# Performance work log

Measured on AMD Instinct MI355X. Metric: run time of the kernel, lower is better.

The kernel has to match this reference:

```python
import jax, jax.numpy as jnp
import numpy as np

N_NODES = 50000
N_USERS = 10000
N_STATE = 1024
N_T1 = 2048
N_T2 = 2048
N_EDGES = 4096


def setup_inputs() -> dict:
    key = jax.random.key(0)
    ks = jax.random.split(key, 10)
    d = N_STATE
    s_u = jax.random.normal(ks[0], (N_USERS, d), jnp.float32)
    x = jax.random.normal(ks[1], (N_NODES, d), jnp.float32)
    # Deterministic graph on which the original torch code is well-defined:
    # POI node 0 has one outgoing edge (edge 0) to tail node 1.
    # Tail node 1 receives edges from heads [0, 2, 3, ..., N_EDGES] in edge order,
    # so list-order in the torch loop aligns with edge-index order.
    heads = np.concatenate([[0], np.arange(2, N_EDGES + 1)]).astype(np.int64)
    tails = np.ones(N_EDGES, dtype=np.int64)
    edge_index = jnp.asarray(np.stack([heads, tails]))
    edge_attr = jax.random.normal(ks[2], (N_EDGES, d), jnp.float32)
    T = jax.random.normal(ks[3], (N_T1, N_T2), jnp.float32)
    u = lambda k, s: jax.random.uniform(k, s, jnp.float32, -1.0, 1.0)
    W_u = u(ks[4], (d, 1))
    W_p = u(ks[5], (d, 1))
    W_T_1 = u(ks[6], (d, N_T1))
    W_T_2 = u(ks[7], (N_T2, 1))
    b_T = u(ks[8], (d, 1))
    W_p_ = u(ks[9], (1, d))
    return dict(s_u=s_u, x=x, edge_attr=edge_attr, T=T, W_u=W_u, W_p=W_p,
                W_T_1=W_T_1, W_T_2=W_T_2, b_T=b_T, W_p_=W_p_,
                edge_index=edge_index, user_index=7, POI_index=0)


def reference(s_u, x, edge_attr, T, W_u, W_p, W_T_1, W_T_2, b_T, W_p_,
              edge_index, user_index, POI_index):
    N, d = x.shape
    heads, tails = edge_index[0], edge_index[1]
    # temporal context vector: sigmoid(W_T_1 @ T @ W_T_2 + b_T), shape (d,)
    t_vec = jax.nn.sigmoid(W_T_1 @ T @ W_T_2 + b_T)[:, 0]
    cur_user = s_u[user_index]   # (d,)
    cur_POI = x[POI_index]       # (d,)
    # user update: u' = sigmoid(u + W_u * (h_P . T'))
    s_u = s_u.at[user_index].set(
        jax.nn.sigmoid(cur_user + W_u[:, 0] * jnp.dot(cur_POI, t_vec)))
    # visited POI update: h' = sigmoid(h + W_p * (u . T'))
    new_POI = jax.nn.sigmoid(cur_POI + W_p[:, 0] * jnp.dot(cur_user, t_vec))
    x = x.at[POI_index].set(new_POI)
    # tail entities of the visited POI: x[tail] = new_POI + edge_attr[e]
    rel_mask = heads == POI_index
    dummy = jnp.zeros((1, d), x.dtype)
    tgt = jnp.where(rel_mask, tails, N)  # route masked-out edges to dummy row
    x = jnp.concatenate([x, dummy], 0).at[tgt].set(new_POI[None, :] + edge_attr)[:N]
    # neighboring POIs: edges whose tail is in the tail set; replicate the original
    # neigh_rel[POI_index] = False / neigh_index.remove(POI_index) pair, which by
    # construction both drop the edge at position POI_index.
    is_tail = jnp.zeros((N + 1,), bool).at[tgt].set(True)[:N]
    neigh_mask = is_tail[tails].at[POI_index].set(False)  # (E,)
    h_emb = x[heads]                        # (E, d), tail-updated embeddings
    scal = (h_emb - edge_attr) @ W_p_[0]    # (E,)  W_p_ . (x[head] - r)
    vals = jax.nn.sigmoid(h_emb + scal[:, None])
    tgt2 = jnp.where(neigh_mask, heads, N)
    x = jnp.concatenate([x, dummy], 0).at[tgt2].set(vals)[:N]
    return (s_u, x)
```

## Files before the change

### kernel.cpp

```cpp
#include <hip/hip_runtime.h>
#include <math.h>
#include <limits.h>

#define D 1024

__device__ __forceinline__ float sigmoidf_(float v) {
    return 1.0f / (1.0f + expf(-v));
}

__device__ __forceinline__ float block_reduce_sum256(float v) {
    #pragma unroll
    for (int off = 32; off; off >>= 1) v += __shfl_down(v, off, 64);
    __shared__ float sm[4];
    int lane = threadIdx.x & 63, w = threadIdx.x >> 6;
    if (lane == 0) sm[w] = v;
    __syncthreads();
    float s = sm[0] + sm[1] + sm[2] + sm[3];
    __syncthreads();
    return s;
}

__device__ __forceinline__ float block_reduce_sum1024(float v) {
    #pragma unroll
    for (int off = 32; off; off >>= 1) v += __shfl_down(v, off, 64);
    __shared__ float sm[16];
    int lane = threadIdx.x & 63, w = threadIdx.x >> 6;
    if (lane == 0) sm[w] = v;
    __syncthreads();
    float s = 0.f;
    #pragma unroll
    for (int i = 0; i < 16; i++) s += sm[i];
    __syncthreads();
    return s;
}

__global__ void k_matvec_T(const float* __restrict__ T,
                           const float* __restrict__ w,
                           float* __restrict__ tmp) {
    int row = blockIdx.x;
    const float4* Tr = (const float4*)(T + (size_t)row * 2048);
    const float4* wv = (const float4*)w;
    float acc = 0.f;
    for (int i = threadIdx.x; i < 512; i += 256) {
        float4 a = Tr[i], b = wv[i];
        acc += a.x * b.x + a.y * b.y + a.z * b.z + a.w * b.w;
    }
    float s = block_reduce_sum256(acc);
    if (threadIdx.x == 0) tmp[row] = s;
}

__global__ void k_tvec(const float* __restrict__ W_T_1,
                       const float* __restrict__ tmp,
                       const float* __restrict__ b_T,
                       float* __restrict__ t_vec) {
    int row = blockIdx.x;
    const float4* Wr = (const float4*)(W_T_1 + (size_t)row * 2048);
    const float4* tv = (const float4*)tmp;
    float acc = 0.f;
    for (int i = threadIdx.x; i < 512; i += 256) {
        float4 a = Wr[i], b = tv[i];
        acc += a.x * b.x + a.y * b.y + a.z * b.z + a.w * b.w;
    }
    float s = block_reduce_sum256(acc);
    if (threadIdx.x == 0) t_vec[row] = sigmoidf_(s + b_T[row]);
}

__global__ void k_setup(const int* __restrict__ edge_index,
                        const float* __restrict__ x,
                        const float* __restrict__ s_u,
                        const float* __restrict__ t_vec,
                        const float* __restrict__ W_u,
                        const float* __restrict__ W_p,
                        const int* __restrict__ user_ptr,
                        const int* __restrict__ POI_ptr,
                        int* __restrict__ tail_edge,
                        int* __restrict__ neigh_edge,
                        float* __restrict__ new_user,
                        float* __restrict__ new_POI, int E) {
    const int tid = threadIdx.x;
    const int POI = POI_ptr[0], user = user_ptr[0];

    for (int e = tid; e < E; e += 1024) {
        int h = edge_index[e], t = edge_index[E + e];
        tail_edge[h] = -1;  tail_edge[t] = -1;
        neigh_edge[h] = -1; neigh_edge[t] = -1;
    }
    if (tid == 0) { tail_edge[POI] = -1; neigh_edge[POI] = -1; }
    __syncthreads();

    for (int e = tid; e < E; e += 1024)
        if (edge_index[e] == POI) atomicMax(&tail_edge[edge_index[E + e]], e);
    __syncthreads();

    for (int e = tid; e < E; e += 1024) {
        if (e == POI) continue;
        int t = edge_index[E + e];
        int te = atomicMax(&tail_edge[t], INT_MIN);
        if (te >= 0) atomicMax(&neigh_edge[edge_index[e]], e);
    }
    __syncthreads();

    float xv = x[(size_t)POI * D + tid];
    float uv = s_u[(size_t)user * D + tid];
    float tv = t_vec[tid];
    float dotP = block_reduce_sum1024(xv * tv);
    float dotU = block_reduce_sum1024(uv * tv);
    new_user[tid] = sigmoidf_(uv + W_u[tid] * dotP);
    new_POI[tid]  = sigmoidf_(xv + W_p[tid] * dotU);
}

__global__ void k_copy_all(const float4* __restrict__ su,
                           const float4* __restrict__ xx,
                           float4* __restrict__ out,
                           int n4_su, int n4_total) {
    int i = blockIdx.x * blockDim.x + threadIdx.x;
    int stride = gridDim.x * blockDim.x;
    for (; i < n4_total; i += stride)
        out[i] = (i < n4_su) ? su[i] : xx[i - n4_su];
}

__global__ void k_fixup(const int* __restrict__ edge_index,
                        const float* __restrict__ edge_attr,
                        const float* __restrict__ x,
                        const float* __restrict__ Wp_row,
                        const float* __restrict__ new_user,
                        const float* __restrict__ new_POI,
                        const int* __restrict__ tail_edge,
                        const int* __restrict__ neigh_edge,
                        const int* __restrict__ user_ptr,
                        const int* __restrict__ POI_ptr,
                        float* __restrict__ out_su,
                        float* __restrict__ out_x, int E) {
    const int e = blockIdx.x;
    const int tid = threadIdx.x;
    const int POI = POI_ptr[0];
    const float4* np_ = (const float4*)new_POI;

    if (e == E) {
        int user = user_ptr[0];
        ((float4*)(out_su + (size_t)user * D))[tid] =
            ((const float4*)new_user)[tid];
        if (tail_edge[POI] < 0 && neigh_edge[POI] < 0)
            ((float4*)(out_x + (size_t)POI * D))[tid] = np_[tid];
        return;
    }

    const int h = edge_index[e], t = edge_index[E + e];

    if (h == POI && tail_edge[t] == e && neigh_edge[t] < 0) {
        const float4* ea = (const float4*)(edge_attr + (size_t)e * D);
        float4 a = np_[tid], b = ea[tid];
        ((float4*)(out_x + (size_t)t * D))[tid] =
            make_float4(a.x + b.x, a.y + b.y, a.z + b.z, a.w + b.w);
    }

    if (e != POI && tail_edge[t] >= 0 && neigh_edge[h] == e) {
        float4 hv;
        int be = tail_edge[h];
        if (be >= 0) {
            const float4* eb = (const float4*)(edge_attr + (size_t)be * D);
            float4 a = np_[tid], b = eb[tid];
            hv = make_float4(a.x + b.x, a.y + b.y, a.z + b.z, a.w + b.w);
        } else if (h == POI) {
            hv = np_[tid];
        } else {
            hv = ((const float4*)(x + (size_t)h * D))[tid];
        }
        const float4* ea = (const float4*)(edge_attr + (size_t)e * D);
        float4 ev = ea[tid];
        float4 w = ((const float4*)Wp_row)[tid];
        float acc = (hv.x - ev.x) * w.x + (hv.y - ev.y) * w.y +
                    (hv.z - ev.z) * w.z + (hv.w - ev.w) * w.w;
        float scal = block_reduce_sum256(acc);
        float4 o;
        o.x = sigmoidf_(hv.x + scal);
        o.y = sigmoidf_(hv.y + scal);
        o.z = sigmoidf_(hv.z + scal);
        o.w = sigmoidf_(hv.w + scal);
        ((float4*)(out_x + (size_t)h * D))[tid] = o;
    }
}

extern "C" void kernel_launch(void* const* d_in, const int* in_sizes, int n_in,
                              void* d_out, int out_size, void* d_ws, size_t ws_size,
                              hipStream_t stream) {
    const float* s_u       = (const float*)d_in[0];
    const float* x         = (const float*)d_in[1];
    const float* edge_attr = (const float*)d_in[2];
    const float* T         = (const float*)d_in[3];
    const float* W_u       = (const float*)d_in[4];
    const float* W_p       = (const float*)d_in[5];
    const float* W_T_1     = (const float*)d_in[6];
    const float* W_T_2     = (const float*)d_in[7];
    const float* b_T       = (const float*)d_in[8];
    const float* W_p_      = (const float*)d_in[9];
    const int*   edge_index = (const int*)d_in[10];
    const int*   user_ptr   = (const int*)d_in[11];
    const int*   POI_ptr    = (const int*)d_in[12];

    const int E       = in_sizes[10] / 2;
    const int N_users = in_sizes[0] / D;
    const int N       = in_sizes[1] / D;

    float* out_su = (float*)d_out;
    float* out_x  = out_su + (size_t)N_users * D;

    float* ws_f      = (float*)d_ws;
    float* tmp       = ws_f;
    float* t_vec     = ws_f + 2048;
    float* new_user  = ws_f + 3072;
    float* new_POI   = ws_f + 4096;
    int*   tail_edge = (int*)(ws_f + 5120);
    int*   neigh_edge = tail_edge + N;

    k_matvec_T<<<2048, 256, 0, stream>>>(T, W_T_2, tmp);
    k_tvec<<<1024, 256, 0, stream>>>(W_T_1, tmp, b_T, t_vec);
    k_setup<<<1, 1024, 0, stream>>>(edge_index, x, s_u, t_vec, W_u, W_p,
                                    user_ptr, POI_ptr, tail_edge, neigh_edge,
                                    new_user, new_POI, E);

    const int n4_su = (int)((size_t)N_users * D / 4);
    const int n4_total = n4_su + (int)((size_t)N * D / 4);
    k_copy_all<<<4096, 256, 0, stream>>>((const float4*)s_u, (const float4*)x,
                                         (float4*)d_out, n4_su, n4_total);

    k_fixup<<<E + 1, 256, 0, stream>>>(edge_index, edge_attr, x, W_p_,
                                       new_user, new_POI, tail_edge, neigh_edge,
                                       user_ptr, POI_ptr, out_su, out_x, E);
}
```

Before: 125.5 us.

## Fuse copy and fixup into a per-row mega kernel, overlap graph setup with matvec

Replaces the separate full-array copy kernel and per-edge fixup kernel with one kernel that handles each output row: it either streams the row with nontemporal loads and stores or computes the updated user, POI, tail or neighbour value in place. This avoids writing special rows twice and removes a launch. The graph-index construction moves into an extra block of the first matvec kernel, and the tail/neighbour tables are initialised with a memset. The POI and user dot products are folded into the t_vec kernel as partial products that each updating block reduces itself. The costs are a per-block branch over 60k rows, redundant recomputation of new_POI in every special row, and a full 2N-int memset.

```diff
diff --git a/kernel.cpp b/kernel.cpp
--- a/kernel.cpp
+++ b/kernel.cpp
@@ -3,6 +3,8 @@
 #include <limits.h>
 
 #define D 1024
+
+typedef float f32x4 __attribute__((ext_vector_type(4)));
 
 __device__ __forceinline__ float sigmoidf_(float v) {
     return 1.0f / (1.0f + expf(-v));
@@ -20,165 +22,153 @@
     return s;
 }
 
-__device__ __forceinline__ float block_reduce_sum1024(float v) {
-    #pragma unroll
-    for (int off = 32; off; off >>= 1) v += __shfl_down(v, off, 64);
-    __shared__ float sm[16];
-    int lane = threadIdx.x & 63, w = threadIdx.x >> 6;
-    if (lane == 0) sm[w] = v;
+__global__ void k_pre(const float* __restrict__ T,
+                      const float* __restrict__ w,
+                      float* __restrict__ tmp,
+                      const int* __restrict__ edge_index,
+                      const int* __restrict__ POI_ptr,
+                      int* __restrict__ tail_edge,
+                      int* __restrict__ neigh_edge,
+                      int n_rows, int E, int t4 ) {
+    const int b = blockIdx.x;
+    const int tid = threadIdx.x;
+    if (b < n_rows) {
+        const float4* Tr = (const float4*)(T + (size_t)b * (size_t)(t4 * 4));
+        const float4* wv = (const float4*)w;
+        float acc = 0.f;
+        for (int i = tid; i < t4; i += 256) {
+            float4 a = Tr[i], c = wv[i];
+            acc += a.x * c.x + a.y * c.y + a.z * c.z + a.w * c.w;
+        }
+        float s = block_reduce_sum256(acc);
+        if (tid == 0) tmp[b] = s;
+        return;
+    }
+    const int POI = POI_ptr[0];
+    for (int e = tid; e < E; e += 256)
+        if (edge_index[e] == POI) atomicMax(&tail_edge[edge_index[E + e]], e);
     __syncthreads();
-    float s = 0.f;
-    #pragma unroll
-    for (int i = 0; i < 16; i++) s += sm[i];
-    __syncthreads();
-    return s;
-}
-
-__global__ void k_matvec_T(const float* __restrict__ T,
-                           const float* __restrict__ w,
-                           float* __restrict__ tmp) {
-    int row = blockIdx.x;
-    const float4* Tr = (const float4*)(T + (size_t)row * 2048);
-    const float4* wv = (const float4*)w;
-    float acc = 0.f;
-    for (int i = threadIdx.x; i < 512; i += 256) {
-        float4 a = Tr[i], b = wv[i];
-        acc += a.x * b.x + a.y * b.y + a.z * b.z + a.w * b.w;
-    }
-    float s = block_reduce_sum256(acc);
-    if (threadIdx.x == 0) tmp[row] = s;
-}
-
-__global__ void k_tvec(const float* __restrict__ W_T_1,
-                       const float* __restrict__ tmp,
-                       const float* __restrict__ b_T,
-                       float* __restrict__ t_vec) {
-    int row = blockIdx.x;
-    const float4* Wr = (const float4*)(W_T_1 + (size_t)row * 2048);
+    for (int e = tid; e < E; e += 256) {
+        if (e == POI) continue;
+        int te = atomicMax(&tail_edge[edge_index[E + e]], INT_MIN);
+        if (te >= 0) atomicMax(&neigh_edge[edge_index[e]], e);
+    }
+}
+
+__global__ void k_tvec2(const float* __restrict__ W_T_1,
+                        const float* __restrict__ tmp,
+                        const float* __restrict__ b_T,
+                        const float* __restrict__ x,
+                        const float* __restrict__ s_u,
+                        const int* __restrict__ user_ptr,
+                        const int* __restrict__ POI_ptr,
+                        float* __restrict__ pu_P,
+                        float* __restrict__ pu_U,
+                        int k4 ) {
+    const int row = blockIdx.x;
+    const float4* Wr = (const float4*)(W_T_1 + (size_t)row * (size_t)(k4 * 4));
     const float4* tv = (const float4*)tmp;
     float acc = 0.f;
-    for (int i = threadIdx.x; i < 512; i += 256) {
-        float4 a = Wr[i], b = tv[i];
-        acc += a.x * b.x + a.y * b.y + a.z * b.z + a.w * b.w;
+    for (int i = threadIdx.x; i < k4; i += 256) {
+        float4 a = Wr[i], c = tv[i];
+        acc += a.x * c.x + a.y * c.y + a.z * c.z + a.w * c.w;
     }
     float s = block_reduce_sum256(acc);
-    if (threadIdx.x == 0) t_vec[row] = sigmoidf_(s + b_T[row]);
-}
-
-__global__ void k_setup(const int* __restrict__ edge_index,
-                        const float* __restrict__ x,
-                        const float* __restrict__ s_u,
-                        const float* __restrict__ t_vec,
-                        const float* __restrict__ W_u,
-                        const float* __restrict__ W_p,
-                        const int* __restrict__ user_ptr,
-                        const int* __restrict__ POI_ptr,
-                        int* __restrict__ tail_edge,
-                        int* __restrict__ neigh_edge,
-                        float* __restrict__ new_user,
-                        float* __restrict__ new_POI, int E) {
+    if (threadIdx.x == 0) {
+        float t = sigmoidf_(s + b_T[row]);
+        pu_P[row] = x[(size_t)POI_ptr[0] * D + row] * t;
+        pu_U[row] = s_u[(size_t)user_ptr[0] * D + row] * t;
+    }
+}
+
+__global__ void k_mega(const float* __restrict__ s_u,
+                       const float* __restrict__ x,
+                       const float* __restrict__ edge_attr,
+                       const float* __restrict__ W_u,
+                       const float* __restrict__ W_p,
+                       const float* __restrict__ Wp_row,
+                       const int* __restrict__ user_ptr,
+                       const int* __restrict__ POI_ptr,
+                       const int* __restrict__ tail_edge,
+                       const int* __restrict__ neigh_edge,
+                       const float* __restrict__ pu_P,
+                       const float* __restrict__ pu_U,
+                       float* __restrict__ out,
+                       int N_users, int E) {
+    const int r = blockIdx.x;
     const int tid = threadIdx.x;
-    const int POI = POI_ptr[0], user = user_ptr[0];
-
-    for (int e = tid; e < E; e += 1024) {
-        int h = edge_index[e], t = edge_index[E + e];
-        tail_edge[h] = -1;  tail_edge[t] = -1;
-        neigh_edge[h] = -1; neigh_edge[t] = -1;
-    }
-    if (tid == 0) { tail_edge[POI] = -1; neigh_edge[POI] = -1; }
-    __syncthreads();
-
-    for (int e = tid; e < E; e += 1024)
-        if (edge_index[e] == POI) atomicMax(&tail_edge[edge_index[E + e]], e);
-    __syncthreads();
-
-    for (int e = tid; e < E; e += 1024) {
-        if (e == POI) continue;
-        int t = edge_index[E + e];
-        int te = atomicMax(&tail_edge[t], INT_MIN);
-        if (te >= 0) atomicMax(&neigh_edge[edge_index[e]], e);
-    }
-    __syncthreads();
-
-    float xv = x[(size_t)POI * D + tid];
-    float uv = s_u[(size_t)user * D + tid];
-    float tv = t_vec[tid];
-    float dotP = block_reduce_sum1024(xv * tv);
-    float dotU = block_reduce_sum1024(uv * tv);
-    new_user[tid] = sigmoidf_(uv + W_u[tid] * dotP);
-    new_POI[tid]  = sigmoidf_(xv + W_p[tid] * dotU);
-}
-
-__global__ void k_copy_all(const float4* __restrict__ su,
-                           const float4* __restrict__ xx,
-                           float4* __restrict__ out,
-                           int n4_su, int n4_total) {
-    int i = blockIdx.x * blockDim.x + threadIdx.x;
-    int stride = gridDim.x * blockDim.x;
-    for (; i < n4_total; i += stride)
-        out[i] = (i < n4_su) ? su[i] : xx[i - n4_su];
-}
-
-__global__ void k_fixup(const int* __restrict__ edge_index,
-                        const float* __restrict__ edge_attr,
-                        const float* __restrict__ x,
-                        const float* __restrict__ Wp_row,
-                        const float* __restrict__ new_user,
-                        const float* __restrict__ new_POI,
-                        const int* __restrict__ tail_edge,
-                        const int* __restrict__ neigh_edge,
-                        const int* __restrict__ user_ptr,
-                        const int* __restrict__ POI_ptr,
-                        float* __restrict__ out_su,
-                        float* __restrict__ out_x, int E) {
-    const int e = blockIdx.x;
-    const int tid = threadIdx.x;
+
+    if (r < N_users) {
+        if (r == user_ptr[0]) {
+            float4 pp = ((const float4*)pu_P)[tid];
+            float dotP = block_reduce_sum256(pp.x + pp.y + pp.z + pp.w);
+            float4 uv = ((const float4*)(s_u + (size_t)r * D))[tid];
+            float4 wu = ((const float4*)W_u)[tid];
+            float4 o;
+            o.x = sigmoidf_(uv.x + wu.x * dotP);
+            o.y = sigmoidf_(uv.y + wu.y * dotP);
+            o.z = sigmoidf_(uv.z + wu.z * dotP);
+            o.w = sigmoidf_(uv.w + wu.w * dotP);
+            ((float4*)(out + (size_t)r * D))[tid] = o;
+        } else {
+            const f32x4* src = (const f32x4*)(s_u + (size_t)r * D);
+            f32x4* dst = (f32x4*)(out + (size_t)r * D);
+            f32x4 v = __builtin_nontemporal_load(&src[tid]);
+            __builtin_nontemporal_store(v, &dst[tid]);
+        }
+        return;
+    }
+
+    const int j = r - N_users;
+    const int ne = neigh_edge[j];
+    const int te = tail_edge[j];
     const int POI = POI_ptr[0];
-    const float4* np_ = (const float4*)new_POI;
-
-    if (e == E) {
-        int user = user_ptr[0];
-        ((float4*)(out_su + (size_t)user * D))[tid] =
-            ((const float4*)new_user)[tid];
-        if (tail_edge[POI] < 0 && neigh_edge[POI] < 0)
-            ((float4*)(out_x + (size_t)POI * D))[tid] = np_[tid];
-        return;
-    }
-
-    const int h = edge_index[e], t = edge_index[E + e];
-
-    if (h == POI && tail_edge[t] == e && neigh_edge[t] < 0) {
-        const float4* ea = (const float4*)(edge_attr + (size_t)e * D);
-        float4 a = np_[tid], b = ea[tid];
-        ((float4*)(out_x + (size_t)t * D))[tid] =
-            make_float4(a.x + b.x, a.y + b.y, a.z + b.z, a.w + b.w);
-    }
-
-    if (e != POI && tail_edge[t] >= 0 && neigh_edge[h] == e) {
-        float4 hv;
-        int be = tail_edge[h];
-        if (be >= 0) {
-            const float4* eb = (const float4*)(edge_attr + (size_t)be * D);
-            float4 a = np_[tid], b = eb[tid];
-            hv = make_float4(a.x + b.x, a.y + b.y, a.z + b.z, a.w + b.w);
-        } else if (h == POI) {
-            hv = np_[tid];
-        } else {
-            hv = ((const float4*)(x + (size_t)h * D))[tid];
-        }
-        const float4* ea = (const float4*)(edge_attr + (size_t)e * D);
-        float4 ev = ea[tid];
-        float4 w = ((const float4*)Wp_row)[tid];
-        float acc = (hv.x - ev.x) * w.x + (hv.y - ev.y) * w.y +
-                    (hv.z - ev.z) * w.z + (hv.w - ev.w) * w.w;
-        float scal = block_reduce_sum256(acc);
-        float4 o;
-        o.x = sigmoidf_(hv.x + scal);
-        o.y = sigmoidf_(hv.y + scal);
-        o.z = sigmoidf_(hv.z + scal);
-        o.w = sigmoidf_(hv.w + scal);
-        ((float4*)(out_x + (size_t)h * D))[tid] = o;
-    }
+
+    if (ne < 0 && te < 0 && j != POI) {
+        const f32x4* src = (const f32x4*)(x + (size_t)j * D);
+        f32x4* dst = (f32x4*)(out + (size_t)r * D);
+        f32x4 v = __builtin_nontemporal_load(&src[tid]);
+        __builtin_nontemporal_store(v, &dst[tid]);
+        return;
+    }
+
+    float4 uu = ((const float4*)pu_U)[tid];
+    float dotU = block_reduce_sum256(uu.x + uu.y + uu.z + uu.w);
+    float4 xp = ((const float4*)(x + (size_t)POI * D))[tid];
+    float4 wp = ((const float4*)W_p)[tid];
+    float4 np;
+    np.x = sigmoidf_(xp.x + wp.x * dotU);
+    np.y = sigmoidf_(xp.y + wp.y * dotU);
+    np.z = sigmoidf_(xp.z + wp.z * dotU);
+    np.w = sigmoidf_(xp.w + wp.w * dotU);
+
+    float4 hv;
+    if (te >= 0) {
+        float4 b = ((const float4*)(edge_attr + (size_t)te * D))[tid];
+        hv = make_float4(np.x + b.x, np.y + b.y, np.z + b.z, np.w + b.w);
+    } else if (j == POI) {
+        hv = np;
+    } else {
+        hv = ((const float4*)(x + (size_t)j * D))[tid];
+    }
+
+    float4* dst = (float4*)(out + (size_t)r * D);
+    if (ne < 0) {
+        dst[tid] = hv;
+        return;
+    }
+
+    float4 ev = ((const float4*)(edge_attr + (size_t)ne * D))[tid];
+    float4 w = ((const float4*)Wp_row)[tid];
+    float acc = (hv.x - ev.x) * w.x + (hv.y - ev.y) * w.y +
+                (hv.z - ev.z) * w.z + (hv.w - ev.w) * w.w;
+    float scal = block_reduce_sum256(acc);
+    float4 o;
+    o.x = sigmoidf_(hv.x + scal);
+    o.y = sigmoidf_(hv.y + scal);
+    o.z = sigmoidf_(hv.z + scal);
+    o.w = sigmoidf_(hv.w + scal);
+    dst[tid] = o;
 }
 
 extern "C" void kernel_launch(void* const* d_in, const int* in_sizes, int n_in,
@@ -201,30 +191,24 @@
     const int E       = in_sizes[10] / 2;
     const int N_users = in_sizes[0] / D;
     const int N       = in_sizes[1] / D;
-
-    float* out_su = (float*)d_out;
-    float* out_x  = out_su + (size_t)N_users * D;
-
-    float* ws_f      = (float*)d_ws;
-    float* tmp       = ws_f;
-    float* t_vec     = ws_f + 2048;
-    float* new_user  = ws_f + 3072;
-    float* new_POI   = ws_f + 4096;
-    int*   tail_edge = (int*)(ws_f + 5120);
+    const int N_T2    = in_sizes[7];
+    const int N_T1    = in_sizes[6] / D;
+
+    float* ws_f       = (float*)d_ws;
+    float* tmp        = ws_f;
+    float* pu_P       = ws_f + N_T1;
+    float* pu_U       = pu_P + D;
+    int*   tail_edge  = (int*)(pu_U + D);
     int*   neigh_edge = tail_edge + N;
 
-    k_matvec_T<<<2048, 256, 0, stream>>>(T, W_T_2, tmp);
-    k_tvec<<<1024, 256, 0, stream>>>(W_T_1, tmp, b_T, t_vec);
-    k_setup<<<1, 1024, 0, stream>>>(edge_index, x, s_u, t_vec, W_u, W_p,
-                                    user_ptr, POI_ptr, tail_edge, neigh_edge,
-                                    new_user, new_POI, E);
-
-    const int n4_su = (int)((size_t)N_users * D / 4);
-    const int n4_total = n4_su + (int)((size_t)N * D / 4);
-    k_copy_all<<<4096, 256, 0, stream>>>((const float4*)s_u, (const float4*)x,
-                                         (float4*)d_out, n4_su, n4_total);
-
-    k_fixup<<<E + 1, 256, 0, stream>>>(edge_index, edge_attr, x, W_p_,
-                                       new_user, new_POI, tail_edge, neigh_edge,
-                                       user_ptr, POI_ptr, out_su, out_x, E);
-}
+    hipMemsetAsync(tail_edge, 0xFF, sizeof(int) * (size_t)(2 * N), stream);
+
+    k_pre<<<N_T1 + 1, 256, 0, stream>>>(T, W_T_2, tmp, edge_index, POI_ptr,
+                                        tail_edge, neigh_edge, N_T1, E, N_T2 / 4);
+    k_tvec2<<<D, 256, 0, stream>>>(W_T_1, tmp, b_T, x, s_u, user_ptr, POI_ptr,
+                                   pu_P, pu_U, N_T1 / 4);
+    k_mega<<<N_users + N, 256, 0, stream>>>(s_u, x, edge_attr, W_u, W_p, W_p_,
+                                            user_ptr, POI_ptr, tail_edge,
+                                            neigh_edge, pu_P, pu_U,
+                                            (float*)d_out, N_users, E);
+}
```

Result: faster. 113.1 us (-9.9%).
